# Kernel optimization log

Measured on AMD Instinct MI355X. Metric: run time of the kernel, lower is better.

The kernel has to match this reference:

```python
import jax, jax.numpy as jnp
import numpy as np

T = 2048        # tokens
HID = 4096      # hidden_size
H = 32          # num attention heads
KV = 8          # num key/value heads (GQA)
D = HID // H    # head_dim = 128
THETA = 10000.0


def setup_inputs() -> dict:
    key = jax.random.key(0)
    k1, k2, k3 = jax.random.split(key, 3)
    hidden_states = jax.random.normal(k1, (T, HID), jnp.float32)
    positions = jnp.arange(T, dtype=jnp.int32)
    Wqkv = jax.random.normal(k2, ((H + 2 * KV) * D, HID), jnp.float32) * 0.02
    Wo = jax.random.normal(k3, (HID, H * D), jnp.float32) * 0.02
    return {"hidden_states": hidden_states, "positions": positions,
            "Wqkv": Wqkv, "Wo": Wo}


def _rope(positions, x):
    """Neox-style rotary embedding. x: [T, h, D], positions: [T]."""
    half = D // 2
    inv_freq = 1.0 / (THETA ** (jnp.arange(half, dtype=jnp.float32) / half))
    ang = positions.astype(jnp.float32)[:, None] * inv_freq      # [T, half]
    cos = jnp.cos(ang)[:, None, :]                                # [T, 1, half]
    sin = jnp.sin(ang)[:, None, :]
    x1, x2 = x[..., :half], x[..., half:]
    return jnp.concatenate([x1 * cos - x2 * sin, x2 * cos + x1 * sin], axis=-1)


def reference(hidden_states, positions, Wqkv, Wo):
    # fused QKV projection (no bias)
    qkv = hidden_states @ Wqkv.T                                  # [T, (H+2KV)*D]
    q, k, v = jnp.split(qkv, [H * D, H * D + KV * D], axis=1)
    q = q.reshape(T, H, D)
    k = k.reshape(T, KV, D)
    v = v.reshape(T, KV, D)
    # RoPE on q and k
    q = _rope(positions, q)
    k = _rope(positions, k)
    # GQA: expand kv heads to match q heads
    g = H // KV
    k = jnp.repeat(k, g, axis=1)                                  # [T, H, D]
    v = jnp.repeat(v, g, axis=1)
    # causal attention (flash-attention math)
    scores = jnp.einsum('thd,shd->hts', q, k) * (D ** -0.5)       # [H, T, T]
    causal = jnp.tril(jnp.ones((T, T), dtype=bool))
    scores = jnp.where(causal[None], scores, jnp.float32(-1e30))
    probs = jax.nn.softmax(scores, axis=-1)
    attn = jnp.einsum('hts,shd->thd', probs, v).reshape(T, H * D)
    # output projection
    return attn @ Wo.T
```

## Files before the change

### kernel.cpp

```cpp
#include <hip/hip_runtime.h>
#include <stdint.h>

#define T_SEQ 2048
#define HIDDEN 4096
#define NHEAD 32
#define NKV 8
#define HDIM 128
#define QKVN 6144

typedef __bf16 bf16x8 __attribute__((ext_vector_type(8)));
typedef float f32x4 __attribute__((ext_vector_type(4)));
typedef unsigned short u16;
typedef u16 u16x8 __attribute__((ext_vector_type(8)));
typedef u16 u16x4 __attribute__((ext_vector_type(4)));

__device__ __forceinline__ u16 f2bf(float f) {
  uint32_t u = __builtin_bit_cast(uint32_t, f);
  u = (u + 0x7fffu + ((u >> 16) & 1u)) >> 16;
  return (u16)u;
}
__device__ __forceinline__ float bf2f(u16 h) {
  uint32_t u = ((uint32_t)h) << 16;
  return __builtin_bit_cast(float, u);
}

__device__ __forceinline__ void gload16(const void* g, void* l) {
  __builtin_amdgcn_global_load_lds(
      (__attribute__((address_space(1))) void*)(uintptr_t)g,
      (__attribute__((address_space(3))) void*)(uintptr_t)l, 16, 0, 0);
}

__global__ void cvt_f32_bf16(const float* __restrict__ in, u16* __restrict__ out, int n) {
  int i = (blockIdx.x * blockDim.x + threadIdx.x) * 4;
  int stride = gridDim.x * blockDim.x * 4;
  for (; i < n; i += stride) {
    float4 v = *(const float4*)(in + i);
    u16x4 o;
    o.x = f2bf(v.x); o.y = f2bf(v.y); o.z = f2bf(v.z); o.w = f2bf(v.w);
    *(u16x4*)(out + i) = o;
  }
}

__global__ void rope_kernel(u16* __restrict__ qkv, const int* __restrict__ pos) {
  int idx = blockIdx.x * blockDim.x + threadIdx.x;
  if (idx >= T_SEQ * 40 * 64) return;
  int i = idx & 63;
  int head = (idx >> 6) % 40;
  int t = idx / (40 * 64);
  int base = head < NHEAD ? head * HDIM : NHEAD * HDIM + (head - NHEAD) * HDIM;
  float p = (float)pos[t];
  float inv_freq = exp2f(-(float)i * (13.287712379549449f / 64.0f));
  float ang = p * inv_freq;
  float s, c;
  sincosf(ang, &s, &c);
  u16* p1 = qkv + (size_t)t * QKVN + base + i;
  u16* p2 = p1 + 64;
  float x1 = bf2f(*p1), x2 = bf2f(*p2);
  *p1 = f2bf(x1 * c - x2 * s);
  *p2 = f2bf(x2 * c + x1 * s);
}

__global__ void vt_kernel(const u16* __restrict__ qkv, u16* __restrict__ vt) {
  __shared__ u16 tile[64][64];
  const int tid = threadIdx.x;
  const int tb = blockIdx.x;
  const int kvh = blockIdx.y >> 1;
  const int d0 = (blockIdx.y & 1) * 64;
  const u16* src = qkv + (size_t)(NHEAD + NKV) * HDIM + kvh * HDIM + d0;
#pragma unroll
  for (int g = 0; g < 2; ++g) {
    int u = g * 256 + tid;
    int t = u >> 3, ds = u & 7;
    u16x8 v = *(const u16x8*)(src + (size_t)(tb * 64 + t) * QKVN + ds * 8);
#pragma unroll
    for (int j = 0; j < 8; ++j) {
      int d = ds * 8 + j;
      tile[d][(((t >> 3) ^ (d & 7)) * 8) + (t & 7)] = v[j];
    }
  }
  __syncthreads();
  u16* dst = vt + ((size_t)kvh * HDIM + d0) * T_SEQ + tb * 64;
#pragma unroll
  for (int g = 0; g < 2; ++g) {
    int u = g * 256 + tid;
    int d = u >> 3, s = u & 7;
    u16x8 v = *(const u16x8*)&tile[d][(s ^ (d & 7)) * 8];
    *(u16x8*)(dst + (size_t)d * T_SEQ + s * 8) = v;
  }
}

__device__ __forceinline__ void storeC(float* p, float v) { *p = v; }
__device__ __forceinline__ void storeC(u16* p, float v) { *p = f2bf(v); }
__device__ __forceinline__ f32x4 mfma16(bf16x8 a, bf16x8 b, f32x4 c) {
  return __builtin_amdgcn_mfma_f32_16x16x32_bf16(a, b, c, 0, 0, 0);
}

template <typename OutT, bool FUSED>
__global__ void __launch_bounds__(512, 2)
gemm256(const u16* __restrict__ A, const u16* __restrict__ B,
        OutT* __restrict__ C0, OutT* __restrict__ C1,
        int N, int K, int NT, int sliceBlocks, int nGemm,
        int nbx, int rw, int rh,
        const float* __restrict__ cvt_in, u16* __restrict__ cvt_out, int cvt_n4) {
  if (FUSED && (int)blockIdx.x >= nGemm) {
    int i = (blockIdx.x - nGemm) * blockDim.x + threadIdx.x;
    int stride = (gridDim.x - nGemm) * blockDim.x;
    for (; i < cvt_n4; i += stride) {
      float4 v = ((const float4*)cvt_in)[i];
      u16x4 o;
      o.x = f2bf(v.x); o.y = f2bf(v.y); o.z = f2bf(v.z); o.w = f2bf(v.w);
      ((u16x4*)cvt_out)[i] = o;
    }
    return;
  }

  __shared__ u16 As_[2][256 * 64];
  __shared__ u16 Bs_[2][256 * 64];

  const int tid = threadIdx.x;
  const int lane = tid & 63;
  const int w = tid >> 6;
  const int wr = w >> 2, wc = w & 3;
  const int l15 = lane & 15, lg = lane >> 4;

  const int bid = blockIdx.x;
  const int slice = bid / sliceBlocks;
  const int wi = bid % sliceBlocks;
  const int k0 = slice * (NT << 6);
  OutT* __restrict__ C = slice ? C1 : C0;

  const int c8 = wi & 7, i8 = wi >> 3;
  const int rpr = nbx / rw;
  const int by = (c8 / rpr) * rh + (i8 % rh);
  const int bx = (c8 % rpr) * rw + (i8 / rh);
  const int bm = by * 256, bn = bx * 256;

  const int u_lo = w * 64 + lane, u_hi = u_lo + 512;
  const int r0 = u_lo >> 3, s0 = (u_lo & 7) ^ (r0 & 7);
  const int r1 = u_hi >> 3, s1 = (u_hi & 7) ^ (r1 & 7);
  const u16* a0s0 = A + (size_t)(bm + r0) * K + k0 + s0 * 8;
  const u16* a0s1 = A + (size_t)(bm + r1) * K + k0 + s1 * 8;
  const u16* a1s0 = A + (size_t)(bm + 128 + r0) * K + k0 + s0 * 8;
  const u16* a1s1 = A + (size_t)(bm + 128 + r1) * K + k0 + s1 * 8;
  const u16* b0s0 = B + (size_t)(bn + r0) * K + k0 + s0 * 8;
  const u16* b0s1 = B + (size_t)(bn + r1) * K + k0 + s1 * 8;
  const u16* b1s0 = B + (size_t)(bn + 128 + r0) * K + k0 + s0 * 8;
  const u16* b1s1 = B + (size_t)(bn + 128 + r1) * K + k0 + s1 * 8;

  const int ax = l15 & 7;
  const int sl0 = (lg ^ ax) * 8;
  const int sl1 = ((4 + lg) ^ ax) * 8;
  const int a_row = (wr * 128 + l15) * 64;
  const int b_row = (wc * 64 + l15) * 64;

  f32x4 acc[8][4] = {};
  bf16x8 bfr[4][2];

#define BARRIER() asm volatile("s_barrier" ::: "memory")
#define WAITBAR(n_) asm volatile("s_waitcnt vmcnt(" #n_ ")\n\ts_barrier" ::: "memory")
#define STAGE_HALF(p0_, p1_, dst_, t_)                                         \
  {                                                                            \
    gload16((p0_) + (size_t)(t_) * 64, (dst_) + (size_t)w * 512);              \
    gload16((p1_) + (size_t)(t_) * 64, (dst_) + 4096 + (size_t)w * 512);       \
  }

  STAGE_HALF(a0s0, a0s1, &As_[0][0], 0);
  STAGE_HALF(a1s0, a1s1, &As_[0][8192], 0);
  STAGE_HALF(b0s0, b0s1, &Bs_[0][0], 0);
  STAGE_HALF(b1s0, b1s1, &Bs_[0][8192], 0);
  STAGE_HALF(b0s0, b0s1, &Bs_[1][0], 1);
  STAGE_HALF(b1s0, b1s1, &Bs_[1][8192], 1);
  WAITBAR(4);

  for (int v = 0; v < NT; ++v) {
    const int cur = v & 1, alt = cur ^ 1;
    const u16* Ac = &As_[cur][0];
    const u16* Bc = &Bs_[cur][0];
    const bool s1ok = (v + 1) < NT, s2ok = (v + 2) < NT;

#define MFMA_QUAD(p_, A0_, A1_, A2_, A3_)                                      \
    __builtin_amdgcn_s_setprio(1);                                             \
    _Pragma("unroll") for (int ni = 0; ni < 4; ++ni) {                         \
      acc[2 * (p_)][ni] = mfma16(A0_, bfr[ni][0], acc[2 * (p_)][ni]);          \
      acc[2 * (p_)][ni] = mfma16(A1_, bfr[ni][1], acc[2 * (p_)][ni]);          \
      acc[2 * (p_) + 1][ni] = mfma16(A2_, bfr[ni][0], acc[2 * (p_) + 1][ni]);  \
      acc[2 * (p_) + 1][ni] = mfma16(A3_, bfr[ni][1], acc[2 * (p_) + 1][ni]);  \
    }                                                                          \
    __builtin_amdgcn_s_setprio(0);

    {
#pragma unroll
      for (int ni = 0; ni < 4; ++ni) {
        bfr[ni][0] = *(const bf16x8*)&Bc[b_row + ni * 1024 + sl0];
        bfr[ni][1] = *(const bf16x8*)&Bc[b_row + ni * 1024 + sl1];
      }
      bf16x8 f0 = *(const bf16x8*)&Ac[a_row + 0 * 1024 + sl0];
      bf16x8 f1 = *(const bf16x8*)&Ac[a_row + 0 * 1024 + sl1];
      bf16x8 f2 = *(const bf16x8*)&Ac[a_row + 1 * 1024 + sl0];
      bf16x8 f3 = *(const bf16x8*)&Ac[a_row + 1 * 1024 + sl1];
      if (s1ok) STAGE_HALF(a0s0, a0s1, &As_[alt][0], v + 1);
      BARRIER();
      MFMA_QUAD(0, f0, f1, f2, f3);
      BARRIER();
    }
    {
      bf16x8 f0 = *(const bf16x8*)&Ac[a_row + 2 * 1024 + sl0];
      bf16x8 f1 = *(const bf16x8*)&Ac[a_row + 2 * 1024 + sl1];
      bf16x8 f2 = *(const bf16x8*)&Ac[a_row + 3 * 1024 + sl0];
      bf16x8 f3 = *(const bf16x8*)&Ac[a_row + 3 * 1024 + sl1];
      if (s1ok) STAGE_HALF(a1s0, a1s1, &As_[alt][8192], v + 1);
      if (s2ok) STAGE_HALF(b0s0, b0s1, &Bs_[cur][0], v + 2);
      BARRIER();
      MFMA_QUAD(1, f0, f1, f2, f3);
      BARRIER();
    }
    {
      bf16x8 f0 = *(const bf16x8*)&Ac[a_row + 4 * 1024 + sl0];
      bf16x8 f1 = *(const bf16x8*)&Ac[a_row + 4 * 1024 + sl1];
      bf16x8 f2 = *(const bf16x8*)&Ac[a_row + 5 * 1024 + sl0];
      bf16x8 f3 = *(const bf16x8*)&Ac[a_row + 5 * 1024 + sl1];
      if (s2ok) STAGE_HALF(b1s0, b1s1, &Bs_[cur][8192], v + 2);
      BARRIER();
      MFMA_QUAD(2, f0, f1, f2, f3);
      BARRIER();
    }
    {
      bf16x8 f0 = *(const bf16x8*)&Ac[a_row + 6 * 1024 + sl0];
      bf16x8 f1 = *(const bf16x8*)&Ac[a_row + 6 * 1024 + sl1];
      bf16x8 f2 = *(const bf16x8*)&Ac[a_row + 7 * 1024 + sl0];
      bf16x8 f3 = *(const bf16x8*)&Ac[a_row + 7 * 1024 + sl1];
      BARRIER();
      MFMA_QUAD(3, f0, f1, f2, f3);
      if (s2ok) { WAITBAR(4); } else { WAITBAR(0); }
    }
#undef MFMA_QUAD
  }

#pragma unroll
  for (int mi = 0; mi < 8; ++mi)
#pragma unroll
    for (int ni = 0; ni < 4; ++ni)
#pragma unroll
      for (int r = 0; r < 4; ++r) {
        int row = bm + wr * 128 + mi * 16 + lg * 4 + r;
        int col = bn + wc * 64 + ni * 16 + l15;
        storeC(&C[(size_t)row * N + col], acc[mi][ni][r]);
      }
#undef STAGE_HALF
#undef WAITBAR
#undef BARRIER
}

__global__ void reduce_add(float* __restrict__ out, const float* __restrict__ part, int n4) {
  int i = blockIdx.x * blockDim.x + threadIdx.x;
  int stride = gridDim.x * blockDim.x;
  for (; i < n4; i += stride) {
    float4 a = ((const float4*)out)[i];
    float4 b = ((const float4*)part)[i];
    a.x += b.x; a.y += b.y; a.z += b.z; a.w += b.w;
    ((float4*)out)[i] = a;
  }
}

__global__ void __launch_bounds__(256, 2)
attn_kernel(const u16* __restrict__ qkv, const u16* __restrict__ vt,
            u16* __restrict__ out) {
  __shared__ u16 Ksh[2][64 * 128];
  __shared__ u16 Vsh[2][128 * 64];
  __shared__ u16 Psh[4][32 * 64];

  const int tid = threadIdx.x;
  const int lane = tid & 63;
  const int w = tid >> 6;
  const int l15 = lane & 15, lg = lane >> 4;

  const int bid = blockIdx.x;
  const int u8 = bid & 255, sfl = bid >> 8;
  const int kvh = u8 & 7;
  const int hg = (u8 >> 3) & 3;
  const int x = (u8 >> 5) & 7;
  const int qi = sfl ? x : (15 - x);
  const int h = kvh * 4 + hg;
  const int q0 = qi * 128;
  const int nt = 2 * qi + 2;
  const int wrow = q0 + w * 32;

  const u16* Kg = qkv + NHEAD * HDIM + kvh * HDIM;
  const u16* Vg = vt + (size_t)kvh * HDIM * T_SEQ;

  bf16x8 qa[2][4];
#pragma unroll
  for (int mi = 0; mi < 2; ++mi) {
    const u16* qrow = qkv + (size_t)(wrow + mi * 16 + l15) * QKVN + h * HDIM + lg * 8;
#pragma unroll
    for (int ks = 0; ks < 4; ++ks) qa[mi][ks] = *(const bf16x8*)(qrow + ks * 32);
  }

  f32x4 acc_o[2][8] = {};
  float m[8], lsum[8];
#pragma unroll
  for (int r = 0; r < 8; ++r) { m[r] = -1e30f; lsum[r] = 0.f; }

  const float scale = 0.088388347648318447f;

#define STAGE_K(kv0, p)                                                        \
  {                                                                            \
    _Pragma("unroll") for (int rnd = 0; rnd < 4; ++rnd) {                      \
      int cc = rnd * 256 + tid;                                                \
      int krow = cc >> 4, kslot = cc & 15;                                     \
      gload16(Kg + (size_t)((kv0) + krow) * QKVN + (kslot ^ (krow & 7)) * 8,   \
              &Ksh[p][(rnd * 256 + w * 64) * 8]);                              \
    }                                                                          \
  }
#define STAGE_V(kv0, p)                                                        \
  {                                                                            \
    _Pragma("unroll") for (int rnd = 0; rnd < 4; ++rnd) {                      \
      int cc = rnd * 256 + tid;                                                \
      int vrow = cc >> 3, ps = cc & 7;                                         \
      gload16(Vg + (size_t)vrow * T_SEQ + (kv0) + ((ps ^ (vrow & 7)) * 8),     \
              &Vsh[p][(rnd * 256 + w * 64) * 8]);                              \
    }                                                                          \
  }

  STAGE_K(0, 0);
  STAGE_V(0, 0);
  __syncthreads();

  for (int t = 0; t < nt; ++t) {
    const int p = t & 1;
    const int kv0 = t * 64;
    const bool more = (t + 1 < nt);
    if (more) {
      STAGE_K(kv0 + 64, p ^ 1);
      STAGE_V(kv0 + 64, p ^ 1);
    }

    if (kv0 <= wrow + 31) {
      f32x4 s[2][4] = {};
#pragma unroll
      for (int ks = 0; ks < 4; ++ks) {
#pragma unroll
        for (int n = 0; n < 4; ++n) {
          int row16 = n * 16 + l15;
          bf16x8 kf = *(const bf16x8*)&Ksh[p][row16 * 128 +
                                              (((ks * 4 + lg) ^ (row16 & 7)) * 8)];
          s[0][n] = mfma16(qa[0][ks], kf, s[0][n]);
          s[1][n] = mfma16(qa[1][ks], kf, s[1][n]);
        }
      }

      const bool diag = (kv0 + 63 > wrow);
      float alpha[8];
#pragma unroll
      for (int mi = 0; mi < 2; ++mi)
#pragma unroll
        for (int r = 0; r < 4; ++r) {
          int ri = mi * 4 + r;
          int tq = wrow + mi * 16 + lg * 4 + r;
          float mx = -1e30f;
#pragma unroll
          for (int n = 0; n < 4; ++n) {
            float v = s[mi][n][r] * scale;
            if (diag && (kv0 + n * 16 + l15) > tq) v = -1e30f;
            s[mi][n][r] = v;
            mx = fmaxf(mx, v);
          }
#pragma unroll
          for (int msk = 1; msk < 16; msk <<= 1) mx = fmaxf(mx, __shfl_xor(mx, msk, 64));
          float mn = fmaxf(m[ri], mx);
          alpha[ri] = __expf(m[ri] - mn);
          m[ri] = mn;
          float ps = 0.f;
#pragma unroll
          for (int n = 0; n < 4; ++n) {
            float pv = __expf(s[mi][n][r] - mn);
            s[mi][n][r] = pv;
            ps += pv;
          }
#pragma unroll
          for (int msk = 1; msk < 16; msk <<= 1) ps += __shfl_xor(ps, msk, 64);
          lsum[ri] = lsum[ri] * alpha[ri] + ps;
          int prow = mi * 16 + lg * 4 + r;
#pragma unroll
          for (int n = 0; n < 4; ++n)
            Psh[w][prow * 64 + (((n * 2 + (l15 >> 3)) ^ (prow & 7)) * 8) + (l15 & 7)] =
                f2bf(s[mi][n][r]);
        }
#pragma unroll
      for (int mi = 0; mi < 2; ++mi)
#pragma unroll
        for (int f = 0; f < 8; ++f)
#pragma unroll
          for (int r = 0; r < 4; ++r) acc_o[mi][f][r] *= alpha[mi * 4 + r];

#pragma unroll
      for (int ks = 0; ks < 2; ++ks) {
        bf16x8 pa0 = *(const bf16x8*)&Psh[w][l15 * 64 + (((ks * 4 + lg) ^ (l15 & 7)) * 8)];
        bf16x8 pa1 = *(const bf16x8*)&Psh[w][(16 + l15) * 64 + (((ks * 4 + lg) ^ (l15 & 7)) * 8)];
#pragma unroll
        for (int nd = 0; nd < 8; ++nd) {
          int d = nd * 16 + l15;
          bf16x8 bv = *(const bf16x8*)&Vsh[p][d * 64 + (((ks * 4 + lg) ^ (d & 7)) * 8)];
          acc_o[0][nd] = mfma16(pa0, bv, acc_o[0][nd]);
          acc_o[1][nd] = mfma16(pa1, bv, acc_o[1][nd]);
        }
      }
    }

    __syncthreads();
  }

#pragma unroll
  for (int mi = 0; mi < 2; ++mi)
#pragma unroll
    for (int nd = 0; nd < 8; ++nd)
#pragma unroll
      for (int r = 0; r < 4; ++r) {
        int row = wrow + mi * 16 + lg * 4 + r;
        int col = h * HDIM + nd * 16 + l15;
        out[(size_t)row * (NHEAD * HDIM) + col] = f2bf(acc_o[mi][nd][r] / lsum[mi * 4 + r]);
      }
#undef STAGE_K
#undef STAGE_V
}

extern "C" void kernel_launch(void* const* d_in, const int* in_sizes, int n_in,
                              void* d_out, int out_size, void* d_ws, size_t ws_size,
                              hipStream_t stream) {
  const float* hs   = (const float*)d_in[0];
  const int*   pos  = (const int*)d_in[1];
  const float* wqkv = (const float*)d_in[2];
  const float* wo   = (const float*)d_in[3];
  float* out = (float*)d_out;
  uint8_t* ws = (uint8_t*)d_ws;

  if (ws_size < 142606336u) return;
  u16* hs_bf   = (u16*)(ws + 0);
  u16* wqkv_bf = (u16*)(ws + 16777216u);
  u16* wo_bf   = (u16*)(ws + 67108864u);
  u16* qkv_bf  = (u16*)(ws + 100663296u);
  u16* attn_bf = (u16*)(ws + 125829120u);
  float* part  = (float*)(ws + 16777216u);
  u16* vt_buf  = (u16*)(ws + 0);

  cvt_f32_bf16<<<2048, 256, 0, stream>>>(hs, hs_bf, T_SEQ * HIDDEN);
  cvt_f32_bf16<<<2048, 256, 0, stream>>>(wqkv, wqkv_bf, QKVN * HIDDEN);

  gemm256<u16, true><<<256, 512, 0, stream>>>(
      hs_bf, wqkv_bf, qkv_bf, qkv_bf, QKVN, HIDDEN, 64,
      192, 192, 24, 3, 8, wo, wo_bf, (HIDDEN * HIDDEN) / 4);

  rope_kernel<<<(T_SEQ * 40 * 64) / 256, 256, 0, stream>>>(qkv_bf, pos);

  vt_kernel<<<dim3(32, 16), 256, 0, stream>>>(qkv_bf, vt_buf);

  attn_kernel<<<512, 256, 0, stream>>>(qkv_bf, vt_buf, attn_bf);

  gemm256<float, false><<<256, 512, 0, stream>>>(
      attn_bf, wo_bf, out, part, HIDDEN, HIDDEN, 32,
      128, 256, 16, 2, 8, nullptr, nullptr, 0);

  reduce_add<<<2048, 256, 0, stream>>>(out, part, (T_SEQ * HIDDEN) / 4);
}
```

Before: 366.5 us.

## Compute transposed S in attention so P stays in registers without LDS round-trip

The QK^T MFMA now takes the operands in swapped order, so each lane holds one query row's scores across the key dimension. Softmax statistics become per-lane with only two cross-lane shuffles, and P can be packed directly into bf16 MFMA A-fragments instead of being written to and reread from shared memory. The V transpose kernel also permutes key order within 64-token blocks to match the register P layout. This removes the Psh LDS traffic and most shuffles, at the cost of extra shuffles to broadcast alpha/lsum and a more complex layout coupling.

```diff
diff --git a/kernel.cpp b/kernel.cpp
--- a/kernel.cpp
+++ b/kernel.cpp
@@ -81,11 +81,13 @@
   __syncthreads();
   u16* dst = vt + ((size_t)kvh * HDIM + d0) * T_SEQ + tb * 64;
 #pragma unroll
-  for (int g = 0; g < 2; ++g) {
+  for (int g = 0; g < 4; ++g) {
     int u = g * 256 + tid;
-    int d = u >> 3, s = u & 7;
-    u16x8 v = *(const u16x8*)&tile[d][(s ^ (d & 7)) * 8];
-    *(u16x8*)(dst + (size_t)d * T_SEQ + s * 8) = v;
+    int d = u >> 4, qd = u & 15;
+    int a = qd >> 3, gg = (qd >> 1) & 3, b = qd & 1;
+    int t0 = 32 * a + 16 * b + 4 * gg;
+    u16x4 v = *(const u16x4*)&tile[d][(((t0 >> 3) ^ (d & 7)) * 8) + (t0 & 7)];
+    *(u16x4*)(dst + (size_t)d * T_SEQ + qd * 4) = v;
   }
 }
 
@@ -267,7 +269,6 @@
             u16* __restrict__ out) {
   __shared__ u16 Ksh[2][64 * 128];
   __shared__ u16 Vsh[2][128 * 64];
-  __shared__ u16 Psh[4][32 * 64];
 
   const int tid = threadIdx.x;
   const int lane = tid & 63;
@@ -297,9 +298,7 @@
   }
 
   f32x4 acc_o[2][8] = {};
-  float m[8], lsum[8];
-#pragma unroll
-  for (int r = 0; r < 8; ++r) { m[r] = -1e30f; lsum[r] = 0.f; }
+  float m[2] = {-1e30f, -1e30f}, lsum[2] = {0.f, 0.f};
 
   const float scale = 0.088388347648318447f;
 
@@ -344,65 +343,83 @@
           int row16 = n * 16 + l15;
           bf16x8 kf = *(const bf16x8*)&Ksh[p][row16 * 128 +
                                               (((ks * 4 + lg) ^ (row16 & 7)) * 8)];
-          s[0][n] = mfma16(qa[0][ks], kf, s[0][n]);
-          s[1][n] = mfma16(qa[1][ks], kf, s[1][n]);
+          s[0][n] = mfma16(kf, qa[0][ks], s[0][n]);
+          s[1][n] = mfma16(kf, qa[1][ks], s[1][n]);
         }
       }
 
       const bool diag = (kv0 + 63 > wrow);
-      float alpha[8];
+      float mx[2];
+#pragma unroll
+      for (int mi = 0; mi < 2; ++mi) {
+        float mm = -1e30f;
+        int tq = wrow + mi * 16 + l15;
+#pragma unroll
+        for (int n = 0; n < 4; ++n)
+#pragma unroll
+          for (int r = 0; r < 4; ++r) {
+            float v = s[mi][n][r] * scale;
+            if (diag && (kv0 + n * 16 + lg * 4 + r) > tq) v = -1e30f;
+            s[mi][n][r] = v;
+            mm = fmaxf(mm, v);
+          }
+        mm = fmaxf(mm, __shfl_xor(mm, 16, 64));
+        mm = fmaxf(mm, __shfl_xor(mm, 32, 64));
+        mx[mi] = mm;
+      }
+
+      float alpha[2];
+#pragma unroll
+      for (int mi = 0; mi < 2; ++mi) {
+        float mn = fmaxf(m[mi], mx[mi]);
+        alpha[mi] = __expf(m[mi] - mn);
+        m[mi] = mn;
+        lsum[mi] *= alpha[mi];
+      }
 #pragma unroll
       for (int mi = 0; mi < 2; ++mi)
 #pragma unroll
         for (int r = 0; r < 4; ++r) {
-          int ri = mi * 4 + r;
-          int tq = wrow + mi * 16 + lg * 4 + r;
-          float mx = -1e30f;
-#pragma unroll
-          for (int n = 0; n < 4; ++n) {
-            float v = s[mi][n][r] * scale;
-            if (diag && (kv0 + n * 16 + l15) > tq) v = -1e30f;
-            s[mi][n][r] = v;
-            mx = fmaxf(mx, v);
-          }
-#pragma unroll
-          for (int msk = 1; msk < 16; msk <<= 1) mx = fmaxf(mx, __shfl_xor(mx, msk, 64));
-          float mn = fmaxf(m[ri], mx);
-          alpha[ri] = __expf(m[ri] - mn);
-          m[ri] = mn;
-          float ps = 0.f;
-#pragma unroll
-          for (int n = 0; n < 4; ++n) {
-            float pv = __expf(s[mi][n][r] - mn);
+          float al = __shfl(alpha[mi], lg * 4 + r, 64);
+#pragma unroll
+          for (int nd = 0; nd < 8; ++nd) acc_o[mi][nd][r] *= al;
+        }
+
+      bf16x8 paf[2][2];
+#pragma unroll
+      for (int mi = 0; mi < 2; ++mi) {
+        float ps = 0.f;
+#pragma unroll
+        for (int n = 0; n < 4; ++n)
+#pragma unroll
+          for (int r = 0; r < 4; ++r) {
+            float pv = __expf(s[mi][n][r] - m[mi]);
             s[mi][n][r] = pv;
             ps += pv;
           }
-#pragma unroll
-          for (int msk = 1; msk < 16; msk <<= 1) ps += __shfl_xor(ps, msk, 64);
-          lsum[ri] = lsum[ri] * alpha[ri] + ps;
-          int prow = mi * 16 + lg * 4 + r;
-#pragma unroll
-          for (int n = 0; n < 4; ++n)
-            Psh[w][prow * 64 + (((n * 2 + (l15 >> 3)) ^ (prow & 7)) * 8) + (l15 & 7)] =
-                f2bf(s[mi][n][r]);
+        ps += __shfl_xor(ps, 16, 64);
+        ps += __shfl_xor(ps, 32, 64);
+        lsum[mi] += ps;
+#pragma unroll
+        for (int ks = 0; ks < 2; ++ks) {
+          u16x8 pk;
+#pragma unroll
+          for (int hn = 0; hn < 2; ++hn)
+#pragma unroll
+            for (int r = 0; r < 4; ++r)
+              pk[hn * 4 + r] = f2bf(s[mi][2 * ks + hn][r]);
+          paf[mi][ks] = __builtin_bit_cast(bf16x8, pk);
         }
-#pragma unroll
-      for (int mi = 0; mi < 2; ++mi)
-#pragma unroll
-        for (int f = 0; f < 8; ++f)
-#pragma unroll
-          for (int r = 0; r < 4; ++r) acc_o[mi][f][r] *= alpha[mi * 4 + r];
+      }
 
 #pragma unroll
       for (int ks = 0; ks < 2; ++ks) {
-        bf16x8 pa0 = *(const bf16x8*)&Psh[w][l15 * 64 + (((ks * 4 + lg) ^ (l15 & 7)) * 8)];
-        bf16x8 pa1 = *(const bf16x8*)&Psh[w][(16 + l15) * 64 + (((ks * 4 + lg) ^ (l15 & 7)) * 8)];
 #pragma unroll
         for (int nd = 0; nd < 8; ++nd) {
           int d = nd * 16 + l15;
           bf16x8 bv = *(const bf16x8*)&Vsh[p][d * 64 + (((ks * 4 + lg) ^ (d & 7)) * 8)];
-          acc_o[0][nd] = mfma16(pa0, bv, acc_o[0][nd]);
-          acc_o[1][nd] = mfma16(pa1, bv, acc_o[1][nd]);
+          acc_o[0][nd] = mfma16(paf[0][ks], bv, acc_o[0][nd]);
+          acc_o[1][nd] = mfma16(paf[1][ks], bv, acc_o[1][nd]);
         }
       }
     }
@@ -413,13 +430,16 @@
 #pragma unroll
   for (int mi = 0; mi < 2; ++mi)
 #pragma unroll
-    for (int nd = 0; nd < 8; ++nd)
-#pragma unroll
-      for (int r = 0; r < 4; ++r) {
-        int row = wrow + mi * 16 + lg * 4 + r;
+    for (int r = 0; r < 4; ++r) {
+      float ls = __shfl(lsum[mi], lg * 4 + r, 64);
+      float inv = 1.f / ls;
+      int row = wrow + mi * 16 + lg * 4 + r;
+#pragma unroll
+      for (int nd = 0; nd < 8; ++nd) {
         int col = h * HDIM + nd * 16 + l15;
-        out[(size_t)row * (NHEAD * HDIM) + col] = f2bf(acc_o[mi][nd][r] / lsum[mi * 4 + r]);
-      }
+        out[(size_t)row * (NHEAD * HDIM) + col] = f2bf(acc_o[mi][nd][r] * inv);
+      }
+    }
 #undef STAGE_K
 #undef STAGE_V
 }
```

Result: faster. 321.1 us (-12.4%).
